# Optimization experiments

Measured on AMD Instinct MI355X. Metric: run time of the kernel, lower is better.

Reference implementation:

```python
import jax, jax.numpy as jnp
import numpy as np

N, E, H, D_IN, D_EDGE, L = 20000, 320000, 128, 128, 32, 4
EPS = 1e-5

def setup_inputs() -> dict:
    key = jax.random.key(0)
    ks = jax.random.split(key, 16)
    d_in_edge = 2 * H + 1 + D_EDGE  # cat[h_row, h_col, radial, edge_attr] (input_nf==hidden here)
    s = 0.02
    inp = {
        'h': jax.random.normal(ks[0], (N, D_IN), jnp.float32),
        'coords': jax.random.normal(ks[1], (N, 3), jnp.float32),
        'edge_attr': jax.random.normal(ks[2], (E, D_EDGE), jnp.float32),
        'edges': jax.random.randint(ks[3], (2, E), 0, N),
        'edge_w1': jax.random.normal(ks[4], (L, d_in_edge, H), jnp.float32) * s,
        'edge_b1': jnp.zeros((L, H), jnp.float32),
        'edge_w2': jax.random.normal(ks[5], (L, H, H), jnp.float32) * s,
        'edge_b2': jnp.zeros((L, H), jnp.float32),
        'node_w1': jax.random.normal(ks[6], (L, H + H, H), jnp.float32) * s,
        'node_b1': jnp.zeros((L, H), jnp.float32),
        'node_w2': jax.random.normal(ks[7], (L, H, H), jnp.float32) * s,
        'node_b2': jnp.zeros((L, H), jnp.float32),
        'ln_g': jnp.ones((H,), jnp.float32),
        'ln_b': jnp.zeros((H,), jnp.float32),
    }
    return inp

def _egnn(h, coords, edge_attr, edges, ew1, eb1, ew2, eb2, nw1, nb1, nw2, nb2, ln_g, ln_b):
    row, col = edges[0], edges[1]
    # squared-distance radial feature; coords are not updated across layers
    # (EGNN.forward discards coordinate updates: h, _, _ = layer(...)).
    diff = coords[row] - coords[col]              # [E,3]
    radial = jnp.sum(diff * diff, axis=-1, keepdims=True)  # [E,1]
    for i in range(L):
        hr, hc = h[row], h[col]                   # gathers [E,H]
        m = jnp.concatenate([hr, hc, radial, edge_attr], axis=-1)
        m = jax.nn.silu(m @ ew1[i] + eb1[i])      # [E,H]
        m = jax.nn.silu(m @ ew2[i] + eb2[i])      # [E,H]
        agg = jax.ops.segment_sum(m, row, num_segments=N)  # scatter-add [N,H]
        z = jnp.concatenate([h, agg], axis=-1)    # [N,2H]
        out = jax.nn.silu(z @ nw1[i] + nb1[i]) @ nw2[i] + nb2[i]
        h = out if i == 0 else h + out            # layer 0 non-recurrent
    mu = jnp.mean(h, axis=-1, keepdims=True)
    var = jnp.mean((h - mu) ** 2, axis=-1, keepdims=True)
    return (h - mu) * jax.lax.rsqrt(var + EPS) * ln_g + ln_b

def reference(h, coords, edge_attr, edges, edge_w1, edge_b1, edge_w2, edge_b2,
              node_w1, node_b1, node_w2, node_b2, ln_g, ln_b):
    return _egnn(h, coords, edge_attr, edges, edge_w1, edge_b1, edge_w2, edge_b2,
                 node_w1, node_b1, node_w2, node_b2, ln_g, ln_b)
```

## Files before the change

kernel.cpp:

```cpp
#include <hip/hip_runtime.h>
#include <hip/hip_bf16.h>

#define NN 20000
#define EE 320000
#define HH 128
#define DE 32
#define LL 4

typedef __bf16 bf16_t;
typedef __bf16 bf16x8 __attribute__((ext_vector_type(8)));
typedef __bf16 bf16x4 __attribute__((ext_vector_type(4)));
typedef float f32x4 __attribute__((ext_vector_type(4)));

static __device__ __forceinline__ float silu_f(float x) {
    return x * __builtin_amdgcn_rcpf(1.f + __expf(-x));
}

static __device__ __forceinline__ int permrow(int el) {
    return ((el >> 2) & 3) * 16 + ((el >> 4) & 3) * 4 + (el & 3);
}

__global__ void prep_weights(const float* __restrict__ ew1, const float* __restrict__ eb1f,
                             const float* __restrict__ ew2,
                             const float* __restrict__ nw1, const float* __restrict__ nw2,
                             bf16_t* __restrict__ WPT, bf16_t* __restrict__ W1C,
                             bf16_t* __restrict__ W2T, bf16_t* __restrict__ N1T,
                             bf16_t* __restrict__ N2T)
{
    int i = blockIdx.x * 256 + threadIdx.x;
    const int SW = LL * 256 * 128;
    if (i < SW) {
        int l = i / (256 * 128), r = i % (256 * 128);
        int c = r / 128, k = r % 128;
        int krow = (c < 128) ? k : 128 + k;
        WPT[i] = (bf16_t)ew1[((size_t)l * 289 + krow) * 128 + (c & 127)];
        return;
    }
    i -= SW;
    const int SC = LL * 128 * 64;
    if (i < SC) {
        int l = i / (128 * 64), r = i % (128 * 64);
        int c = r / 64, kk = r % 64;
        float v;
        if (kk == 0)       v = ew1[((size_t)l * 289 + 256) * 128 + c];
        else if (kk <= 32) v = ew1[((size_t)l * 289 + 256 + kk) * 128 + c];
        else if (kk == 33) v = eb1f[l * 128 + c];
        else               v = 0.f;
        W1C[i] = (bf16_t)v;
        return;
    }
    i -= SC;
    const int S2 = LL * 128 * 128;
    if (i < S2) {
        int l = i / (128 * 128), r = i % (128 * 128);
        int n = r / 128, k = r % 128;
        W2T[i] = (bf16_t)ew2[((size_t)l * 128 + k) * 128 + n];
        return;
    }
    i -= S2;
    const int S3 = LL * 128 * 256;
    if (i < S3) {
        int l = i / (128 * 256), r = i % (128 * 256);
        int n = r / 256, k = r % 256;
        N1T[i] = (bf16_t)nw1[((size_t)l * 256 + k) * 128 + n];
        return;
    }
    i -= S3;
    if (i < S2) {
        int l = i / (128 * 128), r = i % (128 * 128);
        int n = r / 128, k = r % 128;
        N2T[i] = (bf16_t)nw2[((size_t)l * 128 + k) * 128 + n];
    }
}

__global__ void hist_kernel(const int* __restrict__ edges, int* __restrict__ counts)
{
    int e = blockIdx.x * 256 + threadIdx.x;
    if (e < EE) atomicAdd(&counts[edges[e]], 1);
}

__global__ void scan_local(const int* __restrict__ counts, int* __restrict__ cursor,
                           int* __restrict__ bsum)
{
    __shared__ int ws[16];
    const int tid = threadIdx.x;
    const int lane = tid & 63, wv = tid >> 6;
    const int i = blockIdx.x * 1024 + tid;
    int v = (i < NN) ? counts[i] : 0;
    int orig = v;
    #pragma unroll
    for (int off = 1; off < 64; off <<= 1) {
        int t = __shfl_up(v, off);
        if (lane >= off) v += t;
    }
    if (lane == 63) ws[wv] = v;
    __syncthreads();
    if (tid < 16) {
        int s = ws[tid];
        #pragma unroll
        for (int off = 1; off < 16; off <<= 1) {
            int t = __shfl_up(s, off);
            if (tid >= off) s += t;
        }
        ws[tid] = s;
    }
    __syncthreads();
    int waveoff = (wv == 0) ? 0 : ws[wv - 1];
    if (i < NN) cursor[i] = waveoff + v - orig;
    if (tid == 0) bsum[blockIdx.x] = ws[15];
}

__global__ void scan_fixup(int* __restrict__ cursor, const int* __restrict__ bsum)
{
    __shared__ int off;
    const int b = blockIdx.x;
    if (threadIdx.x == 0) {
        int s = 0;
        for (int j = 0; j < b; ++j) s += bsum[j];
        off = s;
    }
    __syncthreads();
    if (b == 0) return;
    int i = b * 1024 + threadIdx.x;
    if (i < NN) cursor[i] += off;
}

__global__ void scatter_build(const int* __restrict__ edges, int* __restrict__ cursor,
                              int* __restrict__ row_s, int* __restrict__ col_s,
                              const float* __restrict__ coords,
                              const float* __restrict__ ea, bf16_t* __restrict__ RE)
{
    int e = blockIdx.x * 256 + threadIdx.x;
    if (e >= EE) return;
    int r = edges[e], c = edges[EE + e];
    int pos = atomicAdd(&cursor[r], 1);
    row_s[pos] = r;
    col_s[pos] = c;
    float dx = coords[r * 3 + 0] - coords[c * 3 + 0];
    float dy = coords[r * 3 + 1] - coords[c * 3 + 1];
    float dz = coords[r * 3 + 2] - coords[c * 3 + 2];
    alignas(16) bf16_t buf[40];
    buf[0] = (bf16_t)(dx * dx + dy * dy + dz * dz);
    #pragma unroll
    for (int j = 0; j < 32; ++j) buf[1 + j] = (bf16_t)ea[(size_t)e * DE + j];
    buf[33] = (bf16_t)1.0f;
    #pragma unroll
    for (int j = 34; j < 40; ++j) buf[j] = (bf16_t)0.f;
    bf16x8* dst = (bf16x8*)(RE + (size_t)pos * 40);
    #pragma unroll
    for (int k = 0; k < 5; ++k) dst[k] = ((const bf16x8*)buf)[k];
}

__global__ __launch_bounds__(256, 2) void node_pre(
    const float* __restrict__ h, const bf16_t* __restrict__ WPT,
    bf16_t* __restrict__ P, int layer)
{
    __shared__ bf16_t Hs[64][136];
    const int tid = threadIdx.x;
    const int n0 = blockIdx.x * 64;
    {
        const int nl = tid >> 2, q = tid & 3;
        const int node = n0 + nl;
        if (node < NN) {
            const float* hp = h + (size_t)node * HH;
            #pragma unroll
            for (int j = 0; j < 8; ++j) {
                float4 v = *(const float4*)(hp + q * 32 + j * 4);
                int k = q * 32 + j * 4;
                Hs[nl][k + 0] = (bf16_t)v.x; Hs[nl][k + 1] = (bf16_t)v.y;
                Hs[nl][k + 2] = (bf16_t)v.z; Hs[nl][k + 3] = (bf16_t)v.w;
            }
        } else {
            #pragma unroll
            for (int j = 0; j < 8; ++j) {
                int k = q * 32 + j * 4;
                Hs[nl][k] = (bf16_t)0.f; Hs[nl][k + 1] = (bf16_t)0.f;
                Hs[nl][k + 2] = (bf16_t)0.f; Hs[nl][k + 3] = (bf16_t)0.f;
            }
        }
    }
    __syncthreads();

    const int lane = tid & 63, w = tid >> 6;
    const int ln = lane & 15, kg = lane >> 4;

    f32x4 acc[4][4] = {};
    const bf16_t* Wl = WPT + (size_t)layer * 256 * 128;
    #pragma unroll
    for (int kt = 0; kt < 4; ++kt) {
        const int kb = kt * 32 + kg * 8;
        bf16x8 a[4], b[4];
        #pragma unroll
        for (int m = 0; m < 4; ++m) a[m] = *(const bf16x8*)&Hs[m * 16 + ln][kb];
        #pragma unroll
        for (int n = 0; n < 4; ++n)
            b[n] = *(const bf16x8*)(Wl + (size_t)(w * 64 + n * 16 + ln) * 128 + kb);
        #pragma unroll
        for (int m = 0; m < 4; ++m)
            #pragma unroll
            for (int n = 0; n < 4; ++n)
                acc[m][n] = __builtin_amdgcn_mfma_f32_16x16x32_bf16(a[m], b[n], acc[m][n], 0, 0, 0);
    }
    #pragma unroll
    for (int n = 0; n < 4; ++n) {
        int col = w * 64 + n * 16 + ln;
        #pragma unroll
        for (int m = 0; m < 4; ++m)
            #pragma unroll
            for (int rr = 0; rr < 4; ++rr) {
                int node = n0 + m * 16 + kg * 4 + rr;
                if (node < NN) P[(size_t)node * 256 + col] = (bf16_t)acc[m][n][rr];
            }
    }
}

__global__ __launch_bounds__(256, 8) void edge_kernel(
    const bf16_t* __restrict__ P, const bf16_t* __restrict__ RE,
    const int* __restrict__ row_s, const int* __restrict__ col_s,
    const bf16_t* __restrict__ W1C, const bf16_t* __restrict__ W2T,
    const float* __restrict__ b2, float* __restrict__ agg, int layer)
{
    __shared__ bf16_t pABs[64][136];

    const int tid = threadIdx.x;
    const int nchunk = gridDim.x >> 3;
    const int swz = (blockIdx.x & 7) * nchunk + (blockIdx.x >> 3);
    const int e0 = swz * 64;

    {
        const int el = tid >> 2, q = tid & 3;
        const int es = e0 + permrow(el);
        int r = row_s[es], c = col_s[es];
        const bf16_t* pa = P + (size_t)r * 256 + q * 32;
        const bf16_t* pb = P + (size_t)c * 256 + 128 + q * 32;
        #pragma unroll
        for (int j = 0; j < 4; ++j) {
            bf16x8 va = *(const bf16x8*)(pa + j * 8);
            bf16x8 vb = *(const bf16x8*)(pb + j * 8);
            bf16x8 o;
            #pragma unroll
            for (int t = 0; t < 8; ++t) o[t] = (bf16_t)((float)va[t] + (float)vb[t]);
            *(bf16x8*)&pABs[el][q * 32 + j * 8] = o;
        }
    }
    __syncthreads();

    const int lane = tid & 63, w = tid >> 6;
    const int ln = lane & 15, kg = lane >> 4;

    f32x4 acc[4][2] = {};
    const bf16_t* W1l = W1C + (size_t)layer * 128 * 64;
    const bf16_t* REbase = RE + (size_t)(e0 + ((ln >> 2) << 4) + (ln & 3)) * 40;
    #pragma unroll
    for (int kt = 0; kt < 2; ++kt) {
        const int kb = kt * 32 + kg * 8;
        bf16x8 a[4], b[2];
        #pragma unroll
        for (int m = 0; m < 4; ++m)
            a[m] = *(const bf16x8*)(REbase + m * 160 + kb);
        #pragma unroll
        for (int n = 0; n < 2; ++n)
            b[n] = *(const bf16x8*)(W1l + (size_t)(w * 32 + n * 16 + ln) * 64 + kb);
        #pragma unroll
        for (int m = 0; m < 4; ++m)
            #pragma unroll
            for (int n = 0; n < 2; ++n)
                acc[m][n] = __builtin_amdgcn_mfma_f32_16x16x32_bf16(a[m], b[n], acc[m][n], 0, 0, 0);
    }

    #pragma unroll
    for (int n = 0; n < 2; ++n) {
        int col = w * 32 + n * 16 + ln;
        #pragma unroll
        for (int m = 0; m < 4; ++m)
            #pragma unroll
            for (int rr = 0; rr < 4; ++rr) {
                int er = m * 16 + kg * 4 + rr;
                float x = acc[m][n][rr] + (float)pABs[er][col];
                pABs[er][col] = (bf16_t)silu_f(x);
            }
    }
    __syncthreads();

    f32x4 acc2[4][2] = {};
    const bf16_t* W2l = W2T + (size_t)layer * 128 * 128;
    #pragma unroll
    for (int kt = 0; kt < 4; ++kt) {
        const int kb = kt * 32 + kg * 8;
        bf16x8 a[4], b[2];
        #pragma unroll
        for (int m = 0; m < 4; ++m) a[m] = *(const bf16x8*)&pABs[m * 16 + ln][kb];
        #pragma unroll
        for (int n = 0; n < 2; ++n)
            b[n] = *(const bf16x8*)(W2l + (size_t)(w * 32 + n * 16 + ln) * 128 + kb);
        #pragma unroll
        for (int m = 0; m < 4; ++m)
            #pragma unroll
            for (int n = 0; n < 2; ++n)
                acc2[m][n] = __builtin_amdgcn_mfma_f32_16x16x32_bf16(a[m], b[n], acc2[m][n], 0, 0, 0);
    }

    {
        int myrow[16];
        {
            const int4* rp = (const int4*)(row_s + e0 + kg * 16);
            #pragma unroll
            for (int j = 0; j < 4; ++j) {
                int4 v = rp[j];
                myrow[j * 4 + 0] = v.x; myrow[j * 4 + 1] = v.y;
                myrow[j * 4 + 2] = v.z; myrow[j * 4 + 3] = v.w;
            }
        }

        #pragma unroll
        for (int n = 0; n < 2; ++n) {
            int col = w * 32 + n * 16 + ln;
            float bias = b2[layer * 128 + col];
            float s = 0.f;
            int cur = myrow[0];
            #pragma unroll
            for (int m = 0; m < 4; ++m) {
                #pragma unroll
                for (int rr = 0; rr < 4; ++rr) {
                    int r = myrow[m * 4 + rr];
                    float v = silu_f(acc2[m][n][rr] + bias);
                    if (r != cur) {
                        atomicAdd(&agg[(size_t)cur * HH + col], s);
                        s = 0.f; cur = r;
                    }
                    s += v;
                }
            }
            atomicAdd(&agg[(size_t)cur * HH + col], s);
        }
    }
}

__global__ __launch_bounds__(256, 2) void node_fused(
    const float* __restrict__ hin, float* __restrict__ hout,
    float* __restrict__ agg,
    const bf16_t* __restrict__ N1T, const float* __restrict__ b1,
    const bf16_t* __restrict__ N2T, const float* __restrict__ b2,
    const bf16_t* __restrict__ WPT, bf16_t* __restrict__ P,
    int layer, int produceP)
{
    __shared__ bf16_t Zs[64][264];
    __shared__ bf16_t M1s[64][136];

    const int tid = threadIdx.x;
    const int n0 = blockIdx.x * 64;

    {
        const int nl = tid >> 2, q = tid & 3;
        const int node = n0 + nl;
        if (node < NN) {
            const float* hp = hin + (size_t)node * HH;
            float* ap = agg + (size_t)node * HH;
            const float4 zero4 = {0.f, 0.f, 0.f, 0.f};
            #pragma unroll
            for (int kk = 0; kk < 64; kk += 4) {
                int k = q * 64 + kk;
                float4 v;
                if (k < 128) {
                    v = *(const float4*)(hp + k);
                } else {
                    v = *(const float4*)(ap + (k - 128));
                    *(float4*)(ap + (k - 128)) = zero4;
                }
                Zs[nl][k + 0] = (bf16_t)v.x; Zs[nl][k + 1] = (bf16_t)v.y;
                Zs[nl][k + 2] = (bf16_t)v.z; Zs[nl][k + 3] = (bf16_t)v.w;
            }
        } else {
            #pragma unroll
            for (int kk = 0; kk < 64; kk += 4) {
                int k = q * 64 + kk;
                Zs[nl][k + 0] = (bf16_t)0.f; Zs[nl][k + 1] = (bf16_t)0.f;
                Zs[nl][k + 2] = (bf16_t)0.f; Zs[nl][k + 3] = (bf16_t)0.f;
            }
        }
    }
    __syncthreads();

    const int lane = tid & 63, w = tid >> 6;
    const int ln = lane & 15, kg = lane >> 4;

    f32x4 acc[2][4] = {};
    const bf16_t* N1l = N1T + (size_t)layer * 128 * 256;
    #pragma unroll
    for (int kt = 0; kt < 8; ++kt) {
        const int kb = kt * 32 + kg * 8;
        bf16x8 aW[2], bZ[4];
        #pragma unroll
        for (int oc = 0; oc < 2; ++oc)
            aW[oc] = *(const bf16x8*)(N1l + (size_t)(w * 32 + oc * 16 + ln) * 256 + kb);
        #pragma unroll
        for (int e = 0; e < 4; ++e) bZ[e] = *(const bf16x8*)&Zs[e * 16 + ln][kb];
        #pragma unroll
        for (int oc = 0; oc < 2; ++oc)
            #pragma unroll
            for (int e = 0; e < 4; ++e)
                acc[oc][e] = __builtin_amdgcn_mfma_f32_16x16x32_bf16(aW[oc], bZ[e], acc[oc][e], 0, 0, 0);
    }

    #pragma unroll
    for (int oc = 0; oc < 2; ++oc) {
        const int ob = w * 32 + oc * 16 + kg * 4;
        const float4 b14 = *(const float4*)&b1[layer * 128 + ob];
        #pragma unroll
        for (int e = 0; e < 4; ++e) {
            const int nd = e * 16 + ln;
            bf16x4 o;
            o[0] = (bf16_t)silu_f(acc[oc][e][0] + b14.x);
            o[1] = (bf16_t)silu_f(acc[oc][e][1] + b14.y);
            o[2] = (bf16_t)silu_f(acc[oc][e][2] + b14.z);
            o[3] = (bf16_t)silu_f(acc[oc][e][3] + b14.w);
            *(bf16x4*)&M1s[nd][ob] = o;
        }
    }
    __syncthreads();

    f32x4 acc2[2][4] = {};
    const bf16_t* N2l = N2T + (size_t)layer * 128 * 128;
    #pragma unroll
    for (int kt = 0; kt < 4; ++kt) {
        const int kb = kt * 32 + kg * 8;
        bf16x8 aW[2], bM[4];
        #pragma unroll
        for (int oc = 0; oc < 2; ++oc)
            aW[oc] = *(const bf16x8*)(N2l + (size_t)(w * 32 + oc * 16 + ln) * 128 + kb);
        #pragma unroll
        for (int e = 0; e < 4; ++e) bM[e] = *(const bf16x8*)&M1s[e * 16 + ln][kb];
        #pragma unroll
        for (int oc = 0; oc < 2; ++oc)
            #pragma unroll
            for (int e = 0; e < 4; ++e)
                acc2[oc][e] = __builtin_amdgcn_mfma_f32_16x16x32_bf16(aW[oc], bM[e], acc2[oc][e], 0, 0, 0);
    }

    #pragma unroll
    for (int oc = 0; oc < 2; ++oc) {
        const int ob = w * 32 + oc * 16 + kg * 4;
        const float4 b24 = *(const float4*)&b2[layer * 128 + ob];
        #pragma unroll
        for (int e = 0; e < 4; ++e) {
            const int ndl = e * 16 + ln;
            const int node = n0 + ndl;
            float x0 = acc2[oc][e][0] + b24.x;
            float x1 = acc2[oc][e][1] + b24.y;
            float x2 = acc2[oc][e][2] + b24.z;
            float x3 = acc2[oc][e][3] + b24.w;
            if (node < NN) {
                if (layer != 0) {
                    float4 hv = *(const float4*)&hin[(size_t)node * HH + ob];
                    x0 += hv.x; x1 += hv.y; x2 += hv.z; x3 += hv.w;
                }
                float4 ov; ov.x = x0; ov.y = x1; ov.z = x2; ov.w = x3;
                *(float4*)&hout[(size_t)node * HH + ob] = ov;
            }
            bf16x4 z;
            z[0] = (bf16_t)x0; z[1] = (bf16_t)x1;
            z[2] = (bf16_t)x2; z[3] = (bf16_t)x3;
            *(bf16x4*)&Zs[ndl][ob] = z;
        }
    }

    if (produceP) {
        __syncthreads();
        f32x4 accP[4][4] = {};
        const bf16_t* Wl = WPT + (size_t)(layer + 1) * 256 * 128;
        #pragma unroll
        for (int kt = 0; kt < 4; ++kt) {
            const int kb = kt * 32 + kg * 8;
            bf16x8 aW[4], bZ[4];
            #pragma unroll
            for (int oc = 0; oc < 4; ++oc)
                aW[oc] = *(const bf16x8*)(Wl + (size_t)(w * 64 + oc * 16 + ln) * 128 + kb);
            #pragma unroll
            for (int e = 0; e < 4; ++e) bZ[e] = *(const bf16x8*)&Zs[e * 16 + ln][kb];
            #pragma unroll
            for (int oc = 0; oc < 4; ++oc)
                #pragma unroll
                for (int e = 0; e < 4; ++e)
                    accP[oc][e] = __builtin_amdgcn_mfma_f32_16x16x32_bf16(aW[oc], bZ[e], accP[oc][e], 0, 0, 0);
        }
        #pragma unroll
        for (int oc = 0; oc < 4; ++oc) {
            const int pb = w * 64 + oc * 16 + kg * 4;
            #pragma unroll
            for (int e = 0; e < 4; ++e) {
                const int node = n0 + e * 16 + ln;
                if (node < NN) {
                    bf16x4 o;
                    o[0] = (bf16_t)accP[oc][e][0]; o[1] = (bf16_t)accP[oc][e][1];
                    o[2] = (bf16_t)accP[oc][e][2]; o[3] = (bf16_t)accP[oc][e][3];
                    *(bf16x4*)&P[(size_t)node * 256 + pb] = o;
                }
            }
        }
    }
}

__global__ void ln_kernel(float* __restrict__ h, const float* __restrict__ g,
                          const float* __restrict__ bb)
{
    int node = blockIdx.x * 4 + (threadIdx.x >> 6);
    int lane = threadIdx.x & 63;
    if (node >= NN) return;
    float* hp = h + (size_t)node * HH;
    float v0 = hp[lane], v1 = hp[lane + 64];
    float s = v0 + v1, sq = v0 * v0 + v1 * v1;
    #pragma unroll
    for (int o = 32; o; o >>= 1) {
        s  += __shfl_xor(s, o);
        sq += __shfl_xor(sq, o);
    }
    float mu  = s * (1.f / 128.f);
    float var = sq * (1.f / 128.f) - mu * mu;
    float inv = rsqrtf(var + 1e-5f);
    hp[lane]      = (v0 - mu) * inv * g[lane]      + bb[lane];
    hp[lane + 64] = (v1 - mu) * inv * g[lane + 64] + bb[lane + 64];
}

extern "C" void kernel_launch(void* const* d_in, const int* in_sizes, int n_in,
                              void* d_out, int out_size, void* d_ws, size_t ws_size,
                              hipStream_t stream)
{
    (void)in_sizes; (void)n_in; (void)out_size; (void)ws_size;

    const float* h_in    = (const float*)d_in[0];
    const float* coords  = (const float*)d_in[1];
    const float* ea      = (const float*)d_in[2];
    const int*   edges   = (const int*)d_in[3];
    const float* ew1     = (const float*)d_in[4];
    const float* eb1     = (const float*)d_in[5];
    const float* ew2     = (const float*)d_in[6];
    const float* eb2     = (const float*)d_in[7];
    const float* nw1     = (const float*)d_in[8];
    const float* nb1     = (const float*)d_in[9];
    const float* nw2     = (const float*)d_in[10];
    const float* nb2     = (const float*)d_in[11];
    const float* ln_g    = (const float*)d_in[12];
    const float* ln_b    = (const float*)d_in[13];

    char* ws = (char*)d_ws;
    int*    counts = (int*)(ws + 0);
    int*    bsum   = (int*)(ws + 80128);
    int*    cursor = (int*)(ws + 160384);
    int*    row_s  = (int*)(ws + 1520512);
    int*    col_s  = (int*)(ws + 2800512);
    bf16_t* RE     = (bf16_t*)(ws + 4080512);
    bf16_t* P      = (bf16_t*)(ws + 29680512);
    float*  agg    = (float*)(ws + 39920512);
    bf16_t* WPT    = (bf16_t*)(ws + 50160512);
    bf16_t* W1C    = (bf16_t*)(ws + 50422656);
    bf16_t* W2T    = (bf16_t*)(ws + 50488192);
    bf16_t* N1T    = (bf16_t*)(ws + 50619264);
    bf16_t* N2T    = (bf16_t*)(ws + 50881408);

    float* h = (float*)d_out;

    prep_weights<<<1664, 256, 0, stream>>>(ew1, eb1, ew2, nw1, nw2,
                                           WPT, W1C, W2T, N1T, N2T);

    hipMemsetAsync(counts, 0, NN * sizeof(int), stream);
    hist_kernel<<<(EE + 255) / 256, 256, 0, stream>>>(edges, counts);
    scan_local<<<(NN + 1023) / 1024, 1024, 0, stream>>>(counts, cursor, bsum);
    scan_fixup<<<(NN + 1023) / 1024, 1024, 0, stream>>>(cursor, bsum);
    scatter_build<<<(EE + 255) / 256, 256, 0, stream>>>(edges, cursor, row_s, col_s,
                                                        coords, ea, RE);

    node_pre<<<(NN + 63) / 64, 256, 0, stream>>>(h_in, WPT, P, 0);

    hipMemsetAsync(agg, 0, (size_t)NN * HH * sizeof(float), stream);

    for (int l = 0; l < LL; ++l) {
        edge_kernel<<<EE / 64, 256, 0, stream>>>(P, RE, row_s, col_s,
                                                 W1C, W2T, eb2, agg, l);
        node_fused<<<(NN + 63) / 64, 256, 0, stream>>>(
            (l == 0) ? h_in : h, h, agg, N1T, nb1, N2T, nb2,
            WPT, P, l, (l < LL - 1) ? 1 : 0);
    }
    ln_kernel<<<NN / 4, 256, 0, stream>>>(h, ln_g, ln_b);
}
```

Baseline: 431.3 us.

## Process two edge tiles per block with register prefetch of next tile's gathers

Each edge block now handles 128 edges as two 64-edge tiles. The second tile's P gathers and RE rows are loaded into registers while the first tile's MFMAs and atomics run, then written to shared memory. RE is also staged through a new shared buffer instead of being read directly from global memory in MFMA layout. The aim is to hide gather latency, at the cost of more registers, lower occupancy (launch bounds 8 to 4), half as many blocks, and the removal of the block swizzle.

```diff
diff --git a/kernel.cpp b/kernel.cpp
--- a/kernel.cpp
+++ b/kernel.cpp
@@ -214,126 +214,165 @@
     }
 }
 
-__global__ __launch_bounds__(256, 8) void edge_kernel(
+__global__ __launch_bounds__(256, 4) void edge_kernel(
     const bf16_t* __restrict__ P, const bf16_t* __restrict__ RE,
     const int* __restrict__ row_s, const int* __restrict__ col_s,
     const bf16_t* __restrict__ W1C, const bf16_t* __restrict__ W2T,
     const float* __restrict__ b2, float* __restrict__ agg, int layer)
 {
     __shared__ bf16_t pABs[64][136];
+    __shared__ bf16_t REb[64][72];
 
     const int tid = threadIdx.x;
-    const int nchunk = gridDim.x >> 3;
-    const int swz = (blockIdx.x & 7) * nchunk + (blockIdx.x >> 3);
-    const int e0 = swz * 64;
-
-    {
-        const int el = tid >> 2, q = tid & 3;
-        const int es = e0 + permrow(el);
-        int r = row_s[es], c = col_s[es];
-        const bf16_t* pa = P + (size_t)r * 256 + q * 32;
-        const bf16_t* pb = P + (size_t)c * 256 + 128 + q * 32;
-        #pragma unroll
-        for (int j = 0; j < 4; ++j) {
-            bf16x8 va = *(const bf16x8*)(pa + j * 8);
-            bf16x8 vb = *(const bf16x8*)(pb + j * 8);
-            bf16x8 o;
-            #pragma unroll
-            for (int t = 0; t < 8; ++t) o[t] = (bf16_t)((float)va[t] + (float)vb[t]);
-            *(bf16x8*)&pABs[el][q * 32 + j * 8] = o;
-        }
-    }
-    __syncthreads();
+    const int el = tid >> 2, q = tid & 3;
+    const int pr = permrow(el);
+    const int e0base = blockIdx.x * 128;
 
     const int lane = tid & 63, w = tid >> 6;
     const int ln = lane & 15, kg = lane >> 4;
 
-    f32x4 acc[4][2] = {};
+    bf16x8 reA = {}, reB = {};
+    bf16x8 va0, va1, va2, va3, vb0, vb1, vb2, vb3;
+
+#define LOADT(E0) do {                                                        \
+        const int es_ = (E0) + pr;                                            \
+        const bf16_t* src_ = RE + (size_t)es_ * 40;                           \
+        if (q == 0)      { reA = *(const bf16x8*)(src_);      reB = *(const bf16x8*)(src_ + 8);  } \
+        else if (q == 1) { reA = *(const bf16x8*)(src_ + 16); reB = *(const bf16x8*)(src_ + 24); } \
+        else if (q == 2) { reA = *(const bf16x8*)(src_ + 32); }               \
+        int r_ = row_s[es_], c_ = col_s[es_];                                 \
+        const bf16_t* pa_ = P + (size_t)r_ * 256 + q * 32;                    \
+        const bf16_t* pb_ = P + (size_t)c_ * 256 + 128 + q * 32;              \
+        va0 = *(const bf16x8*)(pa_);      vb0 = *(const bf16x8*)(pb_);        \
+        va1 = *(const bf16x8*)(pa_ + 8);  vb1 = *(const bf16x8*)(pb_ + 8);    \
+        va2 = *(const bf16x8*)(pa_ + 16); vb2 = *(const bf16x8*)(pb_ + 16);   \
+        va3 = *(const bf16x8*)(pa_ + 24); vb3 = *(const bf16x8*)(pb_ + 24);   \
+    } while (0)
+
+#define ADD8(DST, A, B) do {                                                  \
+        bf16x8 o_;                                                            \
+        _Pragma("unroll")                                                     \
+        for (int t_ = 0; t_ < 8; ++t_) o_[t_] = (bf16_t)((float)(A)[t_] + (float)(B)[t_]); \
+        *(bf16x8*)(DST) = o_;                                                 \
+    } while (0)
+
+#define WRITET(FIRST) do {                                                    \
+        if (q == 0)      { *(bf16x8*)&REb[el][0]  = reA; *(bf16x8*)&REb[el][8]  = reB; } \
+        else if (q == 1) { *(bf16x8*)&REb[el][16] = reA; *(bf16x8*)&REb[el][24] = reB; } \
+        else if (q == 2) { *(bf16x8*)&REb[el][32] = reA;                       \
+                           if (FIRST) { bf16x8 z_ = {}; *(bf16x8*)&REb[el][40] = z_; } } \
+        else if (FIRST)  { bf16x8 z_ = {}; *(bf16x8*)&REb[el][48] = z_;        \
+                           *(bf16x8*)&REb[el][56] = z_; }                      \
+        ADD8(&pABs[el][q * 32 + 0],  va0, vb0);                                \
+        ADD8(&pABs[el][q * 32 + 8],  va1, vb1);                                \
+        ADD8(&pABs[el][q * 32 + 16], va2, vb2);                                \
+        ADD8(&pABs[el][q * 32 + 24], va3, vb3);                                \
+    } while (0)
+
+    LOADT(e0base);
+    WRITET(true);
+    __syncthreads();
+
     const bf16_t* W1l = W1C + (size_t)layer * 128 * 64;
-    const bf16_t* REbase = RE + (size_t)(e0 + ((ln >> 2) << 4) + (ln & 3)) * 40;
-    #pragma unroll
-    for (int kt = 0; kt < 2; ++kt) {
-        const int kb = kt * 32 + kg * 8;
-        bf16x8 a[4], b[2];
-        #pragma unroll
-        for (int m = 0; m < 4; ++m)
-            a[m] = *(const bf16x8*)(REbase + m * 160 + kb);
-        #pragma unroll
-        for (int n = 0; n < 2; ++n)
-            b[n] = *(const bf16x8*)(W1l + (size_t)(w * 32 + n * 16 + ln) * 64 + kb);
-        #pragma unroll
-        for (int m = 0; m < 4; ++m)
+    const bf16_t* W2l = W2T + (size_t)layer * 128 * 128;
+
+    #pragma unroll
+    for (int t = 0; t < 2; ++t) {
+        const int e0 = e0base + t * 64;
+        if (t == 0) LOADT(e0base + 64);
+
+        f32x4 acc[4][2] = {};
+        #pragma unroll
+        for (int kt = 0; kt < 2; ++kt) {
+            const int kb = kt * 32 + kg * 8;
+            bf16x8 a[4], b[2];
+            #pragma unroll
+            for (int m = 0; m < 4; ++m) a[m] = *(const bf16x8*)&REb[m * 16 + ln][kb];
             #pragma unroll
             for (int n = 0; n < 2; ++n)
-                acc[m][n] = __builtin_amdgcn_mfma_f32_16x16x32_bf16(a[m], b[n], acc[m][n], 0, 0, 0);
-    }
-
-    #pragma unroll
-    for (int n = 0; n < 2; ++n) {
-        int col = w * 32 + n * 16 + ln;
-        #pragma unroll
-        for (int m = 0; m < 4; ++m)
-            #pragma unroll
-            for (int rr = 0; rr < 4; ++rr) {
-                int er = m * 16 + kg * 4 + rr;
-                float x = acc[m][n][rr] + (float)pABs[er][col];
-                pABs[er][col] = (bf16_t)silu_f(x);
-            }
-    }
-    __syncthreads();
-
-    f32x4 acc2[4][2] = {};
-    const bf16_t* W2l = W2T + (size_t)layer * 128 * 128;
-    #pragma unroll
-    for (int kt = 0; kt < 4; ++kt) {
-        const int kb = kt * 32 + kg * 8;
-        bf16x8 a[4], b[2];
-        #pragma unroll
-        for (int m = 0; m < 4; ++m) a[m] = *(const bf16x8*)&pABs[m * 16 + ln][kb];
-        #pragma unroll
-        for (int n = 0; n < 2; ++n)
-            b[n] = *(const bf16x8*)(W2l + (size_t)(w * 32 + n * 16 + ln) * 128 + kb);
-        #pragma unroll
-        for (int m = 0; m < 4; ++m)
-            #pragma unroll
-            for (int n = 0; n < 2; ++n)
-                acc2[m][n] = __builtin_amdgcn_mfma_f32_16x16x32_bf16(a[m], b[n], acc2[m][n], 0, 0, 0);
-    }
-
-    {
-        int myrow[16];
-        {
-            const int4* rp = (const int4*)(row_s + e0 + kg * 16);
-            #pragma unroll
-            for (int j = 0; j < 4; ++j) {
-                int4 v = rp[j];
-                myrow[j * 4 + 0] = v.x; myrow[j * 4 + 1] = v.y;
-                myrow[j * 4 + 2] = v.z; myrow[j * 4 + 3] = v.w;
-            }
+                b[n] = *(const bf16x8*)(W1l + (size_t)(w * 32 + n * 16 + ln) * 64 + kb);
+            #pragma unroll
+            for (int m = 0; m < 4; ++m)
+                #pragma unroll
+                for (int n = 0; n < 2; ++n)
+                    acc[m][n] = __builtin_amdgcn_mfma_f32_16x16x32_bf16(a[m], b[n], acc[m][n], 0, 0, 0);
         }
 
         #pragma unroll
         for (int n = 0; n < 2; ++n) {
             int col = w * 32 + n * 16 + ln;
-            float bias = b2[layer * 128 + col];
-            float s = 0.f;
-            int cur = myrow[0];
-            #pragma unroll
-            for (int m = 0; m < 4; ++m) {
+            #pragma unroll
+            for (int m = 0; m < 4; ++m)
                 #pragma unroll
                 for (int rr = 0; rr < 4; ++rr) {
-                    int r = myrow[m * 4 + rr];
-                    float v = silu_f(acc2[m][n][rr] + bias);
-                    if (r != cur) {
-                        atomicAdd(&agg[(size_t)cur * HH + col], s);
-                        s = 0.f; cur = r;
+                    int er = m * 16 + kg * 4 + rr;
+                    float x = acc[m][n][rr] + (float)pABs[er][col];
+                    pABs[er][col] = (bf16_t)silu_f(x);
+                }
+        }
+        __syncthreads();
+
+        f32x4 acc2[4][2] = {};
+        #pragma unroll
+        for (int kt = 0; kt < 4; ++kt) {
+            const int kb = kt * 32 + kg * 8;
+            bf16x8 a[4], b[2];
+            #pragma unroll
+            for (int m = 0; m < 4; ++m) a[m] = *(const bf16x8*)&pABs[m * 16 + ln][kb];
+            #pragma unroll
+            for (int n = 0; n < 2; ++n)
+                b[n] = *(const bf16x8*)(W2l + (size_t)(w * 32 + n * 16 + ln) * 128 + kb);
+            #pragma unroll
+            for (int m = 0; m < 4; ++m)
+                #pragma unroll
+                for (int n = 0; n < 2; ++n)
+                    acc2[m][n] = __builtin_amdgcn_mfma_f32_16x16x32_bf16(a[m], b[n], acc2[m][n], 0, 0, 0);
+        }
+
+        {
+            int myrow[16];
+            {
+                const int4* rp = (const int4*)(row_s + e0 + kg * 16);
+                #pragma unroll
+                for (int j = 0; j < 4; ++j) {
+                    int4 v = rp[j];
+                    myrow[j * 4 + 0] = v.x; myrow[j * 4 + 1] = v.y;
+                    myrow[j * 4 + 2] = v.z; myrow[j * 4 + 3] = v.w;
+                }
+            }
+
+            #pragma unroll
+            for (int n = 0; n < 2; ++n) {
+                int col = w * 32 + n * 16 + ln;
+                float bias = b2[layer * 128 + col];
+                float s = 0.f;
+                int cur = myrow[0];
+                #pragma unroll
+                for (int m = 0; m < 4; ++m) {
+                    #pragma unroll
+                    for (int rr = 0; rr < 4; ++rr) {
+                        int r = myrow[m * 4 + rr];
+                        float v = silu_f(acc2[m][n][rr] + bias);
+                        if (r != cur) {
+                            atomicAdd(&agg[(size_t)cur * HH + col], s);
+                            s = 0.f; cur = r;
+                        }
+                        s += v;
                     }
-                    s += v;
                 }
-            }
-            atomicAdd(&agg[(size_t)cur * HH + col], s);
-        }
-    }
+                atomicAdd(&agg[(size_t)cur * HH + col], s);
+            }
+        }
+
+        if (t == 0) {
+            __syncthreads();
+            WRITET(false);
+            __syncthreads();
+        }
+    }
+#undef LOADT
+#undef ADD8
+#undef WRITET
 }
 
 __global__ __launch_bounds__(256, 2) void node_fused(
@@ -574,8 +613,8 @@
     hipMemsetAsync(agg, 0, (size_t)NN * HH * sizeof(float), stream);
 
     for (int l = 0; l < LL; ++l) {
-        edge_kernel<<<EE / 64, 256, 0, stream>>>(P, RE, row_s, col_s,
-                                                 W1C, W2T, eb2, agg, l);
+        edge_kernel<<<EE / 128, 256, 0, stream>>>(P, RE, row_s, col_s,
+                                                  W1C, W2T, eb2, agg, l);
         node_fused<<<(NN + 63) / 64, 256, 0, stream>>>(
             (l == 0) ? h_in : h, h, agg, N1T, nb1, N2T, nb2,
             WPT, P, l, (l < LL - 1) ? 1 : 0);
```

Result: slower. 508.5 us (+17.9%).
